# Kernel optimization log

Hardware: AMD Instinct MI355X
Metric: run time of the kernel (lower is better)

## Reference

```python
import jax, jax.numpy as jnp
import numpy as np

INPUT_DIM = 1024
OUTPUT_DIM = 1024
DEGREE = 8
N_TOKENS = 8192


def setup_inputs() -> dict:
    key = jax.random.key(0)
    k1, k2 = jax.random.split(key)
    x = jax.random.normal(k1, (N_TOKENS, INPUT_DIM), dtype=jnp.float32)
    # xavier_normal_ with gain = 1/(input_dim*(degree+1)) over fan dims (output_dim, degree+1)
    fan_in, fan_out = OUTPUT_DIM, DEGREE + 1  # torch treats dim0/dim1 as fans; scale is tiny anyway
    gain = 1.0 / (INPUT_DIM * (DEGREE + 1))
    std = gain * np.sqrt(2.0 / (INPUT_DIM + OUTPUT_DIM))
    cheby_coeffs = std * jax.random.normal(k2, (INPUT_DIM, OUTPUT_DIM, DEGREE + 1), dtype=jnp.float32)
    return {"x": x, "cheby_coeffs": cheby_coeffs}


def reference(x, cheby_coeffs):
    # x: (..., input_dim) -> y: (..., output_dim)
    degree_p1 = cheby_coeffs.shape[-1]
    theta = jnp.arccos(jnp.tanh(x))                      # (..., i)
    arange = jnp.arange(degree_p1, dtype=x.dtype)        # (d,)
    basis = jnp.cos(theta[..., None] * arange)           # (..., i, d) Chebyshev T_d(tanh(x))
    y = jnp.einsum('...id,iod->...o', basis, cheby_coeffs)
    return y
```

## Files before the change

### kernel.cpp

```cpp
#include <hip/hip_runtime.h>


typedef __bf16 bf16;
typedef __bf16 bf16x8 __attribute__((ext_vector_type(8)));
typedef float f32x2 __attribute__((ext_vector_type(2)));
typedef float f32x4 __attribute__((ext_vector_type(4)));
typedef float f32x16 __attribute__((ext_vector_type(16)));

#define MFMA __builtin_amdgcn_mfma_f32_32x32x16_bf16

__device__ __forceinline__ void g2lds16(const void* g, void* l) {
  __builtin_amdgcn_global_load_lds(
      (const __attribute__((address_space(1))) unsigned int*)g,
      (__attribute__((address_space(3))) unsigned int*)l, 16, 0, 0);
}

__device__ __forceinline__ float fast_tanh(float a) {
  float e = __expf(a + a);
  return 1.f - 2.f * __builtin_amdgcn_rcpf(e + 1.f);
}

__global__ __launch_bounds__(256)
void cheby_prep4(const float* __restrict__ x, const float* __restrict__ C,
                 bf16* __restrict__ A, bf16* __restrict__ B,
                 float* __restrict__ bias_p) {
  const int bid = blockIdx.x, tid = threadIdx.x;
  if (bid < 2048) {
    __shared__ float xs[64][65];
    const int rb = bid >> 4, ig = bid & 15;
    #pragma unroll
    for (int it = 0; it < 4; ++it) {
      const int e = tid + it * 256;
      const int rr = e >> 4, c4 = (e & 15) * 4;
      f32x4 v = *(const f32x4*)(x + (size_t)(rb * 64 + rr) * 1024 + ig * 64 + c4);
      xs[rr][c4 + 0] = v.x; xs[rr][c4 + 1] = v.y;
      xs[rr][c4 + 2] = v.z; xs[rr][c4 + 3] = v.w;
    }
    __syncthreads();
    const int rl = tid & 63, ih = tid >> 6;
    const int mb = rb >> 1;
    const int rs = (rb & 1) * 64 + rl;
    const int m32 = rs >> 5, ml = rs & 31;
    bf16* aout = A + (size_t)mb * 1048576;
    #pragma unroll
    for (int q = 0; q < 4; ++q) {
      #pragma unroll
      for (int j = 0; j < 4; ++j) {
        const int il = ih * 16 + q * 4 + j;
        const int ia = ig * 64 + il;
        const int kt = ia >> 3, cc = ia & 7;
        float z = fast_tanh(xs[rl][il]);
        float z2 = z + z, pv = 1.f, cv = z;
        bf16x8 v;
        #pragma unroll
        for (int d = 0; d < 8; ++d) {
          v[d] = (bf16)cv;
          float nx = z2 * cv - pv; pv = cv; cv = nx;
        }
        const int widx = (((cc >> 1) * 4 + m32) * 2 + (cc & 1)) * 32 + ml;
        *(bf16x8*)(aout + (size_t)kt * 8192 + widx * 8) = v;
      }
    }
    return;
  }
  const int b2 = bid - 2048;
  __shared__ float tile[32][292];
  const int i0 = (b2 >> 5) * 32, o0 = (b2 & 31) * 32;
  {
    const int r = tid >> 3, seg = tid & 7;
    const float* src = C + (size_t)(i0 + r) * 9216 + (size_t)o0 * 9 + seg * 36;
    float* dst = &tile[r][seg * 36];
    #pragma unroll
    for (int v = 0; v < 9; ++v) *(f32x4*)(dst + v * 4) = *(const f32x4*)(src + v * 4);
  }
  __syncthreads();
  #pragma unroll
  for (int j = 0; j < 4; ++j) {
    int e = tid + 256 * j;
    int il = e >> 5, ol = e & 31;
    int i = i0 + il, o = o0 + ol;
    bf16x8 v;
    #pragma unroll
    for (int d = 0; d < 8; ++d) v[d] = (bf16)tile[il][ol * 9 + 1 + d];
    const int cc = i & 7;
    size_t tnum = (size_t)(o >> 7) * 128 + (i >> 3);
    const int widx = (((cc >> 1) * 4 + ((o & 127) >> 5)) * 2 + (cc & 1)) * 32 + (o & 31);
    *(bf16x8*)(B + tnum * 8192 + widx * 8) = v;
  }
  if (tid < 32) {
    float s = 0.f;
    #pragma unroll
    for (int i = 0; i < 32; ++i) s += tile[i][tid * 9];
    bias_p[(size_t)(b2 >> 5) * 1024 + o0 + tid] = s;
  }
}

__global__ __launch_bounds__(512, 1)
void cheby_gemm5(const bf16* __restrict__ A, const bf16* __restrict__ B,
                 const float* __restrict__ bias_p, float* __restrict__ out) {
  __shared__ bf16 ring[3][24576];
  const int tid = threadIdx.x;
  const int lane = tid & 63, w = tid >> 6;
  const int wm = w >> 1, wn = w & 1;
  const int bid = blockIdx.x;
  const int wgid = (bid & 7) * 32 + (bid >> 3);
  const int mb2 = wgid >> 3, nb = wgid & 7;

  const int ml = lane & 31, h = lane >> 5;
  const int aLane = h * 256 + ml * 8;
  const int row0 = wm * 64, row1 = row0 + 32;
  const int aBase0 = (row0 >> 7) * 8192 + ((row0 >> 5) & 3) * 512 + aLane;
  const int aBase1 = (row1 >> 7) * 8192 + ((row1 >> 5) & 3) * 512 + aLane;
  const int bBase  = 16384 + wn * 1024 + aLane;

  const bf16* aG = A + (size_t)(mb2 * 2) * 1048576 + tid * 8;
  const bf16* bG = B + (size_t)nb * 1048576 + tid * 8;

  f32x16 acc[2][2];
  #pragma unroll
  for (int a = 0; a < 2; ++a)
    #pragma unroll
    for (int b = 0; b < 2; ++b)
      #pragma unroll
      for (int r = 0; r < 16; ++r) acc[a][b][r] = 0.f;

  struct F { bf16x8 a0[4], a1[4], b0[4], b1[4]; };
  F f0, f1;

  auto issueB6 = [&](int t, int p) {
    g2lds16(aG + (size_t)t * 8192,                  &ring[p][tid * 8]);
    g2lds16(aG + (size_t)t * 8192 + 4096,           &ring[p][4096 + tid * 8]);
    g2lds16(aG + 1048576 + (size_t)t * 8192,        &ring[p][8192 + tid * 8]);
    g2lds16(aG + 1048576 + (size_t)t * 8192 + 4096, &ring[p][12288 + tid * 8]);
    g2lds16(bG + (size_t)t * 8192,                  &ring[p][16384 + tid * 8]);
    g2lds16(bG + (size_t)t * 8192 + 4096,           &ring[p][20480 + tid * 8]);
  };
  auto loadFrags = [&](F& f, const bf16* ra) {
    #pragma unroll
    for (int ks = 0; ks < 4; ++ks) {
      const int off = (ks & 1) * 2048 + (ks >> 1) * 4096;
      f.a0[ks] = *(const bf16x8*)(ra + aBase0 + off);
      f.a1[ks] = *(const bf16x8*)(ra + aBase1 + off);
      f.b0[ks] = *(const bf16x8*)(ra + bBase + off);
      f.b1[ks] = *(const bf16x8*)(ra + bBase + off + 512);
    }
  };
  auto mfma16 = [&](F& c) {
    __builtin_amdgcn_s_setprio(1);
    #pragma unroll
    for (int ks = 0; ks < 4; ++ks) {
      acc[0][0] = MFMA(c.a0[ks], c.b0[ks], acc[0][0], 0, 0, 0);
      acc[0][1] = MFMA(c.a0[ks], c.b1[ks], acc[0][1], 0, 0, 0);
      acc[1][0] = MFMA(c.a1[ks], c.b0[ks], acc[1][0], 0, 0, 0);
      acc[1][1] = MFMA(c.a1[ks], c.b1[ks], acc[1][1], 0, 0, 0);
    }
    __builtin_amdgcn_s_setprio(0);
  };

  issueB6(0, 0); issueB6(1, 1); issueB6(2, 2);
  asm volatile("s_waitcnt vmcnt(6)" ::: "memory");
  __builtin_amdgcn_s_barrier();
  loadFrags(f0, &ring[0][0]);
  asm volatile("s_waitcnt lgkmcnt(0)" ::: "memory");
  __builtin_amdgcn_s_barrier();

  auto step = [&](int t, int bufI, int bufR, F& cur, F& nxt, bool rd) {
    if (t + 3 < 128) issueB6(t + 3, bufI);
    if (rd) loadFrags(nxt, &ring[bufR][0]);
    mfma16(cur);
    asm volatile("s_waitcnt lgkmcnt(0)" ::: "memory");
    if (t < 125) asm volatile("s_waitcnt vmcnt(6)" ::: "memory");
    else         asm volatile("s_waitcnt vmcnt(0)" ::: "memory");
    __builtin_amdgcn_s_barrier();
  };

  #pragma unroll 1
  for (int t6 = 0; t6 < 126; t6 += 6) {
    step(t6 + 0, 0, 1, f0, f1, true);
    step(t6 + 1, 1, 2, f1, f0, true);
    step(t6 + 2, 2, 0, f0, f1, true);
    step(t6 + 3, 0, 1, f1, f0, true);
    step(t6 + 4, 1, 2, f0, f1, true);
    step(t6 + 5, 2, 0, f1, f0, true);
  }
  step(126, 0, 1, f0, f1, true);
  step(127, 1, 2, f1, f0, false);

  const int c0 = nb * 128 + wn * 64 + ml;
  float bv0 = 0.f, bv1 = 0.f;
  #pragma unroll
  for (int p = 0; p < 32; ++p) {
    bv0 += bias_p[(size_t)p * 1024 + c0];
    bv1 += bias_p[(size_t)p * 1024 + c0 + 32];
  }
  const int r0 = mb2 * 256 + wm * 64;
  #pragma unroll
  for (int mt = 0; mt < 2; ++mt)
    #pragma unroll
    for (int r = 0; r < 16; ++r) {
      int row = r0 + mt * 32 + (r & 3) + 8 * (r >> 2) + 4 * h;
      float* po = out + (size_t)row * 1024 + c0;
      po[0]  = acc[mt][0][r] + bv0;
      po[32] = acc[mt][1][r] + bv1;
    }
}

__global__ __launch_bounds__(256)
void cheby_naive(const float* __restrict__ x, const float* __restrict__ C,
                 float* __restrict__ out) {
  const int t = blockIdx.x, tid = threadIdx.x;
  float acc[4] = {0.f, 0.f, 0.f, 0.f};
  for (int i = 0; i < 1024; ++i) {
    float th = tanhf(x[(size_t)t * 1024 + i]);
    float T[9]; T[0] = 1.f; T[1] = th;
    #pragma unroll
    for (int d = 2; d < 9; ++d) T[d] = 2.f * th * T[d - 1] - T[d - 2];
    #pragma unroll
    for (int j = 0; j < 4; ++j) {
      const float* cp = &C[((size_t)i * 1024 + tid + j * 256) * 9];
      float s = 0.f;
      #pragma unroll
      for (int d = 0; d < 9; ++d) s += T[d] * cp[d];
      acc[j] += s;
    }
  }
  #pragma unroll
  for (int j = 0; j < 4; ++j) out[(size_t)t * 1024 + tid + j * 256] = acc[j];
}

extern "C" void kernel_launch(void* const* d_in, const int* in_sizes, int n_in,
                              void* d_out, int out_size, void* d_ws, size_t ws_size,
                              hipStream_t stream) {
  (void)in_sizes; (void)n_in; (void)out_size;
  const float* x = (const float*)d_in[0];
  const float* C = (const float*)d_in[1];
  float* out = (float*)d_out;

  const size_t a_bytes  = (size_t)8192 * 8192 * 2;
  const size_t b_bytes  = (size_t)8 * 128 * 8192 * 2;
  const size_t bp_bytes = (size_t)32 * 1024 * 4;

  if (ws_size >= a_bytes + b_bytes + bp_bytes) {
    bf16*  A      = (bf16*)d_ws;
    bf16*  B      = (bf16*)((char*)d_ws + a_bytes);
    float* bias_p = (float*)((char*)d_ws + a_bytes + b_bytes);
    cheby_prep4<<<3072, 256, 0, stream>>>(x, C, A, B, bias_p);
    cheby_gemm5<<<256, 512, 0, stream>>>(A, B, bias_p, out);
  } else {
    cheby_naive<<<8192, 256, 0, stream>>>(x, C, out);
  }
}
```

Measured before the change: 250.1 us.

## Generate Chebyshev basis inside GEMM from tanh values instead of materializing A

```diff
diff --git a/kernel.cpp b/kernel.cpp
--- a/kernel.cpp
+++ b/kernel.cpp
@@ -21,49 +21,25 @@
 }
 
 __global__ __launch_bounds__(256)
-void cheby_prep4(const float* __restrict__ x, const float* __restrict__ C,
-                 bf16* __restrict__ A, bf16* __restrict__ B,
-                 float* __restrict__ bias_p) {
+void cheby_prep5(const float* __restrict__ x, const float* __restrict__ C,
+                 bf16* __restrict__ B, float* __restrict__ bias_p,
+                 float* __restrict__ th2) {
   const int bid = blockIdx.x, tid = threadIdx.x;
-  if (bid < 2048) {
-    __shared__ float xs[64][65];
-    const int rb = bid >> 4, ig = bid & 15;
-    #pragma unroll
-    for (int it = 0; it < 4; ++it) {
-      const int e = tid + it * 256;
-      const int rr = e >> 4, c4 = (e & 15) * 4;
-      f32x4 v = *(const f32x4*)(x + (size_t)(rb * 64 + rr) * 1024 + ig * 64 + c4);
-      xs[rr][c4 + 0] = v.x; xs[rr][c4 + 1] = v.y;
-      xs[rr][c4 + 2] = v.z; xs[rr][c4 + 3] = v.w;
-    }
-    __syncthreads();
-    const int rl = tid & 63, ih = tid >> 6;
-    const int mb = rb >> 1;
-    const int rs = (rb & 1) * 64 + rl;
-    const int m32 = rs >> 5, ml = rs & 31;
-    bf16* aout = A + (size_t)mb * 1048576;
-    #pragma unroll
-    for (int q = 0; q < 4; ++q) {
-      #pragma unroll
-      for (int j = 0; j < 4; ++j) {
-        const int il = ih * 16 + q * 4 + j;
-        const int ia = ig * 64 + il;
-        const int kt = ia >> 3, cc = ia & 7;
-        float z = fast_tanh(xs[rl][il]);
-        float z2 = z + z, pv = 1.f, cv = z;
-        bf16x8 v;
-        #pragma unroll
-        for (int d = 0; d < 8; ++d) {
-          v[d] = (bf16)cv;
-          float nx = z2 * cv - pv; pv = cv; cv = nx;
-        }
-        const int widx = (((cc >> 1) * 4 + m32) * 2 + (cc & 1)) * 32 + ml;
-        *(bf16x8*)(aout + (size_t)kt * 8192 + widx * 8) = v;
-      }
-    }
+  if (bid < 4096) {
+    const int g = bid * 256 + tid;
+    const int r = g >> 7, i0 = (g & 127) * 8;
+    const float* xp = x + (size_t)r * 1024 + i0;
+    f32x4 v0 = *(const f32x4*)(xp);
+    f32x4 v1 = *(const f32x4*)(xp + 4);
+    f32x4 e, o;
+    e.x = fast_tanh(v0.x); e.y = fast_tanh(v0.z); e.z = fast_tanh(v1.x); e.w = fast_tanh(v1.z);
+    o.x = fast_tanh(v0.y); o.y = fast_tanh(v0.w); o.z = fast_tanh(v1.y); o.w = fast_tanh(v1.w);
+    float* dp = th2 + (size_t)r * 1024 + i0;
+    *(f32x4*)(dp)     = e;
+    *(f32x4*)(dp + 4) = o;
     return;
   }
-  const int b2 = bid - 2048;
+  const int b2 = bid - 4096;
   __shared__ float tile[32][292];
   const int i0 = (b2 >> 5) * 32, o0 = (b2 & 31) * 32;
   {
@@ -96,9 +72,9 @@
 }
 
 __global__ __launch_bounds__(512, 1)
-void cheby_gemm5(const bf16* __restrict__ A, const bf16* __restrict__ B,
+void cheby_gemm6(const float* __restrict__ th2, const bf16* __restrict__ B,
                  const float* __restrict__ bias_p, float* __restrict__ out) {
-  __shared__ bf16 ring[3][24576];
+  __shared__ bf16 ring[3][12288];
   const int tid = threadIdx.x;
   const int lane = tid & 63, w = tid >> 6;
   const int wm = w >> 1, wn = w & 1;
@@ -107,14 +83,12 @@
   const int mb2 = wgid >> 3, nb = wgid & 7;
 
   const int ml = lane & 31, h = lane >> 5;
-  const int aLane = h * 256 + ml * 8;
-  const int row0 = wm * 64, row1 = row0 + 32;
-  const int aBase0 = (row0 >> 7) * 8192 + ((row0 >> 5) & 3) * 512 + aLane;
-  const int aBase1 = (row1 >> 7) * 8192 + ((row1 >> 5) & 3) * 512 + aLane;
-  const int bBase  = 16384 + wn * 1024 + aLane;
-
-  const bf16* aG = A + (size_t)(mb2 * 2) * 1048576 + tid * 8;
-  const bf16* bG = B + (size_t)nb * 1048576 + tid * 8;
+  const int bBase = wn * 1024 + h * 256 + ml * 8;
+  const int row0 = wm * 64;
+  const int sIdx = (row0 + ml) * 8 + h * 4;
+
+  const bf16*  bG = B   + (size_t)nb * 1048576 + tid * 8;
+  const float* tG = th2 + (size_t)(mb2 * 256 + (tid >> 1)) * 1024 + (tid & 1) * 4;
 
   f32x16 acc[2][2];
   #pragma unroll
@@ -124,67 +98,85 @@
       #pragma unroll
       for (int r = 0; r < 16; ++r) acc[a][b][r] = 0.f;
 
-  struct F { bf16x8 a0[4], a1[4], b0[4], b1[4]; };
-  F f0, f1;
-
-  auto issueB6 = [&](int t, int p) {
-    g2lds16(aG + (size_t)t * 8192,                  &ring[p][tid * 8]);
-    g2lds16(aG + (size_t)t * 8192 + 4096,           &ring[p][4096 + tid * 8]);
-    g2lds16(aG + 1048576 + (size_t)t * 8192,        &ring[p][8192 + tid * 8]);
-    g2lds16(aG + 1048576 + (size_t)t * 8192 + 4096, &ring[p][12288 + tid * 8]);
-    g2lds16(bG + (size_t)t * 8192,                  &ring[p][16384 + tid * 8]);
-    g2lds16(bG + (size_t)t * 8192 + 4096,           &ring[p][20480 + tid * 8]);
-  };
-  auto loadFrags = [&](F& f, const bf16* ra) {
+  bf16x8 afr0[2][4], afr1[2][4];
+  bf16x8 bfr0[2][4], bfr1[2][4];
+
+  auto issue3 = [&](int t, int p) {
+    g2lds16(bG + (size_t)t * 8192,        &ring[p][tid * 8]);
+    g2lds16(bG + (size_t)t * 8192 + 4096, &ring[p][4096 + tid * 8]);
+    g2lds16(tG + (size_t)t * 8,           &ring[p][8192 + tid * 8]);
+  };
+  auto loadBF = [&](bf16x8 (&bf)[2][4], const bf16* ra) {
     #pragma unroll
     for (int ks = 0; ks < 4; ++ks) {
-      const int off = (ks & 1) * 2048 + (ks >> 1) * 4096;
-      f.a0[ks] = *(const bf16x8*)(ra + aBase0 + off);
-      f.a1[ks] = *(const bf16x8*)(ra + aBase1 + off);
-      f.b0[ks] = *(const bf16x8*)(ra + bBase + off);
-      f.b1[ks] = *(const bf16x8*)(ra + bBase + off + 512);
-    }
-  };
-  auto mfma16 = [&](F& c) {
+      bf[0][ks] = *(const bf16x8*)(ra + bBase + ks * 2048);
+      bf[1][ks] = *(const bf16x8*)(ra + bBase + ks * 2048 + 512);
+    }
+  };
+  auto gen = [&](bf16x8 (&dst)[2][4], const bf16* ra) {
+    const float* thL = (const float*)(ra + 8192);
+    f32x4 s0 = *(const f32x4*)(thL + sIdx);
+    f32x4 s1 = *(const f32x4*)(thL + sIdx + 256);
+    #pragma unroll
+    for (int ks = 0; ks < 4; ++ks) {
+      f32x2 t  = {s0[ks], s1[ks]};
+      f32x2 t2 = t + t;
+      f32x2 prev = {1.f, 1.f}, cur = t;
+      #pragma unroll
+      for (int j = 0; j < 8; ++j) {
+        dst[0][ks][j] = (bf16)cur.x;
+        dst[1][ks][j] = (bf16)cur.y;
+        f32x2 nx = t2 * cur - prev;
+        prev = cur; cur = nx;
+      }
+    }
+  };
+  auto mfma16 = [&](bf16x8 (&af)[2][4], bf16x8 (&bf)[2][4]) {
     __builtin_amdgcn_s_setprio(1);
     #pragma unroll
     for (int ks = 0; ks < 4; ++ks) {
-      acc[0][0] = MFMA(c.a0[ks], c.b0[ks], acc[0][0], 0, 0, 0);
-      acc[0][1] = MFMA(c.a0[ks], c.b1[ks], acc[0][1], 0, 0, 0);
-      acc[1][0] = MFMA(c.a1[ks], c.b0[ks], acc[1][0], 0, 0, 0);
-      acc[1][1] = MFMA(c.a1[ks], c.b1[ks], acc[1][1], 0, 0, 0);
+      acc[0][0] = MFMA(af[0][ks], bf[0][ks], acc[0][0], 0, 0, 0);
+      acc[0][1] = MFMA(af[0][ks], bf[1][ks], acc[0][1], 0, 0, 0);
+      acc[1][0] = MFMA(af[1][ks], bf[0][ks], acc[1][0], 0, 0, 0);
+      acc[1][1] = MFMA(af[1][ks], bf[1][ks], acc[1][1], 0, 0, 0);
     }
     __builtin_amdgcn_s_setprio(0);
   };
 
-  issueB6(0, 0); issueB6(1, 1); issueB6(2, 2);
+  issue3(0, 0); issue3(1, 1); issue3(2, 2);
   asm volatile("s_waitcnt vmcnt(6)" ::: "memory");
   __builtin_amdgcn_s_barrier();
-  loadFrags(f0, &ring[0][0]);
+  loadBF(bfr0, &ring[0][0]);
+  gen(afr0, &ring[0][0]);
   asm volatile("s_waitcnt lgkmcnt(0)" ::: "memory");
   __builtin_amdgcn_s_barrier();
 
-  auto step = [&](int t, int bufI, int bufR, F& cur, F& nxt, bool rd) {
-    if (t + 3 < 128) issueB6(t + 3, bufI);
-    if (rd) loadFrags(nxt, &ring[bufR][0]);
-    mfma16(cur);
+  auto step = [&](int t, int pI, int pR,
+                  bf16x8 (&curA)[2][4], bf16x8 (&curB)[2][4],
+                  bf16x8 (&nxtA)[2][4], bf16x8 (&nxtB)[2][4], bool rd) {
+    if (t + 3 < 128) issue3(t + 3, pI);
+    if (rd) {
+      loadBF(nxtB, &ring[pR][0]);
+      gen(nxtA, &ring[pR][0]);
+    }
+    mfma16(curA, curB);
     asm volatile("s_waitcnt lgkmcnt(0)" ::: "memory");
-    if (t < 125) asm volatile("s_waitcnt vmcnt(6)" ::: "memory");
+    if (t < 125) asm volatile("s_waitcnt vmcnt(3)" ::: "memory");
     else         asm volatile("s_waitcnt vmcnt(0)" ::: "memory");
     __builtin_amdgcn_s_barrier();
   };
 
   #pragma unroll 1
   for (int t6 = 0; t6 < 126; t6 += 6) {
-    step(t6 + 0, 0, 1, f0, f1, true);
-    step(t6 + 1, 1, 2, f1, f0, true);
-    step(t6 + 2, 2, 0, f0, f1, true);
-    step(t6 + 3, 0, 1, f1, f0, true);
-    step(t6 + 4, 1, 2, f0, f1, true);
-    step(t6 + 5, 2, 0, f1, f0, true);
-  }
-  step(126, 0, 1, f0, f1, true);
-  step(127, 1, 2, f1, f0, false);
+    step(t6 + 0, 0, 1, afr0, bfr0, afr1, bfr1, true);
+    step(t6 + 1, 1, 2, afr1, bfr1, afr0, bfr0, true);
+    step(t6 + 2, 2, 0, afr0, bfr0, afr1, bfr1, true);
+    step(t6 + 3, 0, 1, afr1, bfr1, afr0, bfr0, true);
+    step(t6 + 4, 1, 2, afr0, bfr0, afr1, bfr1, true);
+    step(t6 + 5, 2, 0, afr1, bfr1, afr0, bfr0, true);
+  }
+  step(126, 0, 1, afr0, bfr0, afr1, bfr1, true);
+  step(127, 1, 2, afr1, bfr1, afr0, bfr0, false);
 
   const int c0 = nb * 128 + wn * 64 + ml;
   float bv0 = 0.f, bv1 = 0.f;
@@ -236,16 +228,16 @@
   const float* C = (const float*)d_in[1];
   float* out = (float*)d_out;
 
-  const size_t a_bytes  = (size_t)8192 * 8192 * 2;
   const size_t b_bytes  = (size_t)8 * 128 * 8192 * 2;
   const size_t bp_bytes = (size_t)32 * 1024 * 4;
-
-  if (ws_size >= a_bytes + b_bytes + bp_bytes) {
-    bf16*  A      = (bf16*)d_ws;
-    bf16*  B      = (bf16*)((char*)d_ws + a_bytes);
-    float* bias_p = (float*)((char*)d_ws + a_bytes + b_bytes);
-    cheby_prep4<<<3072, 256, 0, stream>>>(x, C, A, B, bias_p);
-    cheby_gemm5<<<256, 512, 0, stream>>>(A, B, bias_p, out);
+  const size_t th_bytes = (size_t)8192 * 1024 * 4;
+
+  if (ws_size >= b_bytes + bp_bytes + th_bytes) {
+    bf16*  B      = (bf16*)d_ws;
+    float* bias_p = (float*)((char*)d_ws + b_bytes);
+    float* th2    = (float*)((char*)d_ws + b_bytes + bp_bytes);
+    cheby_prep5<<<5120, 256, 0, stream>>>(x, C, B, bias_p, th2);
+    cheby_gemm6<<<256, 512, 0, stream>>>(th2, B, bias_p, out);
   } else {
     cheby_naive<<<8192, 256, 0, stream>>>(x, C, out);
   }
```

Result: slower. 371.4 us (+48.5%).
